# Kernel tuning notes

Hardware: AMD Instinct MI355X
Metric: run time of the kernel (lower is better)

## Reference

```python
import jax, jax.numpy as jnp
import numpy as np

B, H, W, C = 16, 192, 192, 128   # batch, height, width, d_inner
R = 16      # lora_rank (bottleneck width between lora_down and lora_up)
RK = 8      # internal LoRA rank = lora_rank // 2
NC = 5      # cache_size
SCALE = 1.0 / RK        # alpha / rank with alpha = 1.0
THRESH = 0.7            # similarity_threshold
EPS = 1e-8              # torch cosine_similarity eps


def _lora_paths(x, A1, B1, A2, B2):
    # lora_down: C -> RK -> R, lora_up: R -> RK -> C, each scaled by 1/RK (dropout off in eval)
    down = ((x @ A1) @ B1) * SCALE          # [B,H,W,R]
    up = ((down @ A2) @ B2) * SCALE         # [B,H,W,C]
    return down, up


def setup_inputs() -> dict:
    key = jax.random.key(0)
    ks = jax.random.split(key, 9)
    x = jax.random.normal(ks[0], (B, H, W, C), dtype=jnp.float32)
    A1 = (jax.random.normal(ks[1], (C, RK)) / np.sqrt(C)).astype(jnp.float32)
    B1 = (jax.random.normal(ks[2], (RK, R)) / np.sqrt(RK)).astype(jnp.float32)
    A2 = (jax.random.normal(ks[3], (R, RK)) / np.sqrt(R)).astype(jnp.float32)
    B2 = (jax.random.normal(ks[4], (RK, C)) / np.sqrt(RK)).astype(jnp.float32)
    W1 = (jax.random.normal(ks[5], (C + R, C)) / np.sqrt(C + R)).astype(jnp.float32)
    b1 = jnp.zeros((C,), dtype=jnp.float32)
    W2 = (jax.random.normal(ks[6], (C, C)) / np.sqrt(C)).astype(jnp.float32)
    b2 = jnp.zeros((C,), dtype=jnp.float32)
    cache_w = jnp.array(0.5, dtype=jnp.float32)
    # Build cache entries as noisy copies of x_lora[:NC] so the first NC batch
    # elements clear the 0.7 cosine threshold (fused branch) and the rest do not.
    _, xl = _lora_paths(x, A1, B1, A2, B2)
    noise = jax.random.normal(ks[7], (NC, H, W, C), dtype=jnp.float32) * (0.05 * jnp.std(xl))
    cache_feats = xl[:NC] + noise           # [NC,H,W,C]
    return {"x": x, "A1": A1, "B1": B1, "A2": A2, "B2": B2,
            "W1": W1, "b1": b1, "W2": W2, "b2": b2,
            "cache_w": cache_w, "cache_feats": cache_feats}


def reference(x, A1, B1, A2, B2, W1, b1, W2, b2, cache_w, cache_feats):
    down, x_lora = _lora_paths(x, A1, B1, A2, B2)   # [B,H,W,R], [B,H,W,C]
    # Per-channel cosine similarity over the HW axis, averaged over channels
    num = jnp.einsum('bhwc,nhwc->bnc', x_lora, cache_feats)        # [B,NC,C]
    xn = jnp.sqrt(jnp.sum(x_lora * x_lora, axis=(1, 2)))           # [B,C]
    cn = jnp.sqrt(jnp.sum(cache_feats * cache_feats, axis=(1, 2))) # [NC,C]
    denom = jnp.maximum(xn[:, None, :], EPS) * jnp.maximum(cn[None, :, :], EPS)
    sims = jnp.mean(num / denom, axis=-1)                          # [B,NC]
    best_idx = jnp.argmax(sims, axis=1)                            # first max, like list.index
    best_sim = jnp.max(sims, axis=1)
    best = cache_feats[best_idx]                                   # [B,H,W,C]
    # Gated blend with cached feature, then fusion MLP on concat([blend, lora_down])
    cw = jax.nn.sigmoid(cache_w)
    blend = cw * x_lora + (1.0 - cw) * best
    h = jnp.concatenate([blend, down], axis=-1) @ W1 + b1          # [B,H,W,C]
    fused = jax.nn.silu(h) @ W2 + b2
    mask = (best_sim > THRESH)[:, None, None, None]
    return jnp.where(mask, fused, x_lora)
```

## Files before the change

kernel.cpp:

```cpp
#include <hip/hip_runtime.h>
#include <math.h>

#define BATCH 16
#define HWPIX 36864
#define CCH 128
#define NCACHE 5
#define SCALE 0.125f
#define THRESH 0.7f
#define EPSV 1e-8f

typedef _Float16 f16;
typedef __attribute__((ext_vector_type(8))) _Float16 f16x8;
typedef __attribute__((ext_vector_type(4))) float f32x4;

__global__ __launch_bounds__(256) void kpre1(
    const float* __restrict__ A1, const float* __restrict__ B1,
    const float* __restrict__ A2, const float* __restrict__ B2,
    const float* __restrict__ W1, const float* __restrict__ W2,
    const float* __restrict__ cache_w,
    float* __restrict__ M1f, float* __restrict__ M12f,
    f16* __restrict__ M12h, f16* __restrict__ Qh, f16* __restrict__ W2h) {
  __shared__ float M1s[128 * 16];
  __shared__ float M2s[16 * 128];
  int t = threadIdx.x;
  int blk = blockIdx.x;
  for (int idx = t; idx < 2048; idx += 256) {
    int i = idx >> 4, r = idx & 15;
    float s = 0.f;
    for (int k = 0; k < 8; ++k) s += A1[i * 8 + k] * B1[k * 16 + r];
    s *= SCALE;
    M1s[idx] = s;
    if (blk == 0) M1f[idx] = s;
  }
  for (int idx = t; idx < 2048; idx += 256) {
    int r = idx >> 7, j = idx & 127;
    float s = 0.f;
    for (int k = 0; k < 8; ++k) s += A2[r * 8 + k] * B2[k * 128 + j];
    M2s[idx] = s * SCALE;
  }
  __syncthreads();
  for (int idx = blk * 2048 + t; idx < blk * 2048 + 2048; idx += 256) {
    int i = idx >> 7, j = idx & 127;
    float s = 0.f;
    for (int r = 0; r < 16; ++r) s += M1s[i * 16 + r] * M2s[r * 128 + j];
    M12f[idx] = s;
    M12h[(((i >> 3) * 128 + j) << 3) + (i & 7)] = (f16)s;
  }
  float cw = 1.f / (1.f + __expf(-cache_w[0]));
  float qs = 1.f - cw;
  for (int idx = blk * 2048 + t; idx < blk * 2048 + 2048; idx += 256) {
    int k = idx >> 7, n = idx & 127;
    int ci = (((k >> 3) * 128 + n) << 3) + (k & 7);
    Qh[ci] = (f16)(qs * W1[k * 128 + n]);
    W2h[ci] = (f16)W2[k * 128 + n];
  }
}

__global__ __launch_bounds__(256) void kpre2(
    const float* __restrict__ W1, const float* __restrict__ M1f,
    const float* __restrict__ M12f, const float* __restrict__ cache_w,
    f16* __restrict__ Ph) {
  int t = threadIdx.x;
  int k = blockIdx.x * 8 + (t >> 5);
  int n0 = (t & 31) * 4;
  float cw = 1.f / (1.f + __expf(-cache_w[0]));
  float sa[4] = {0, 0, 0, 0}, sb[4] = {0, 0, 0, 0};
  for (int tt = 0; tt < 128; ++tt) {
    float m = M12f[k * 128 + tt];
    const float* wr = &W1[tt * 128 + n0];
    sa[0] += m * wr[0]; sa[1] += m * wr[1]; sa[2] += m * wr[2]; sa[3] += m * wr[3];
  }
  for (int r = 0; r < 16; ++r) {
    float m = M1f[k * 16 + r];
    const float* wr = &W1[(128 + r) * 128 + n0];
    sb[0] += m * wr[0]; sb[1] += m * wr[1]; sb[2] += m * wr[2]; sb[3] += m * wr[3];
  }
  for (int u = 0; u < 4; ++u) {
    int n = n0 + u;
    Ph[(((k >> 3) * 128 + n) << 3) + (k & 7)] = (f16)(cw * sa[u] + sb[u]);
  }
}

__global__ __launch_bounds__(256, 3) void k2(
    const float* __restrict__ x, const float* __restrict__ cache,
    const f16* __restrict__ M12h, float* __restrict__ out,
    float* __restrict__ num, float* __restrict__ xn2, float* __restrict__ cn2) {
  __shared__ f16 Bs[16 * 128 * 8];
  __shared__ f16 XLb[64 * 132];
  int t = threadIdx.x;
  int chunk = blockIdx.x;
  int grp = blockIdx.y;
  long pb = (long)chunk * 64;
  {
    const uint4* src = (const uint4*)M12h;
    uint4* dst = (uint4*)Bs;
    for (int i = t; i < 2048; i += 256) dst[i] = src[i];
  }
  int lane = t & 63, w = t >> 6, l15 = lane & 15, q = lane >> 4;
  int arow = w * 16 + l15;
  int c = t & 127;
  bool hi = t >= 128;
  __syncthreads();

  for (int g = 0; g < 8; ++g) {
    int b = grp * 8 + g;
    const float* xb = x + ((long)b * HWPIX + pb) * CCH;
    f32x4 acc[8];
#pragma unroll
    for (int ni = 0; ni < 8; ++ni) acc[ni] = 0;
#pragma unroll
    for (int kk = 0; kk < 4; ++kk) {
      const float* ap = xb + arow * CCH + kk * 32 + q * 8;
      f32x4 a0 = *(const f32x4*)ap;
      f32x4 a1 = *(const f32x4*)(ap + 4);
      f16x8 a;
      a[0] = (f16)a0[0]; a[1] = (f16)a0[1]; a[2] = (f16)a0[2]; a[3] = (f16)a0[3];
      a[4] = (f16)a1[0]; a[5] = (f16)a1[1]; a[6] = (f16)a1[2]; a[7] = (f16)a1[3];
#pragma unroll
      for (int ni = 0; ni < 8; ++ni) {
        f16x8 bb = *(const f16x8*)&Bs[(((kk * 4 + q) * 128 + ni * 16 + l15)) << 3];
        acc[ni] = __builtin_amdgcn_mfma_f32_16x16x32_f16(a, bb, acc[ni], 0, 0, 0);
      }
    }
    __syncthreads();
    float* ob = out + ((long)b * HWPIX + pb) * CCH;
#pragma unroll
    for (int ni = 0; ni < 8; ++ni) {
      int cc = ni * 16 + l15;
#pragma unroll
      for (int r = 0; r < 4; ++r) {
        int p = w * 16 + q * 4 + r;
        float v = acc[ni][r];
        ob[(long)p * CCH + cc] = v;
        XLb[p * 132 + cc] = (f16)v;
      }
    }
    __syncthreads();
    {
      bool docn = (grp == 0) && (g == 0);
      const float* cb = cache + pb * CCH + c;
      float s0 = 0, s1 = 0, s2v = 0;
      float q0 = 0, q1 = 0, q2 = 0;
      if (!hi) {
#pragma unroll 4
        for (int p = 0; p < 64; ++p) {
          float xl = (float)XLb[p * 132 + c];
          float cv0 = cb[((long)0 * HWPIX + p) * CCH];
          float cv1 = cb[((long)1 * HWPIX + p) * CCH];
          float cv2 = cb[((long)2 * HWPIX + p) * CCH];
          s0 += xl * cv0; s1 += xl * cv1; s2v += xl * cv2;
          if (docn) { q0 += cv0 * cv0; q1 += cv1 * cv1; q2 += cv2 * cv2; }
        }
        atomicAdd(&num[((long)b * 5 + 0) * 128 + c], s0);
        atomicAdd(&num[((long)b * 5 + 1) * 128 + c], s1);
        atomicAdd(&num[((long)b * 5 + 2) * 128 + c], s2v);
        if (docn) {
          atomicAdd(&cn2[0 * 128 + c], q0);
          atomicAdd(&cn2[1 * 128 + c], q1);
          atomicAdd(&cn2[2 * 128 + c], q2);
        }
      } else {
#pragma unroll 4
        for (int p = 0; p < 64; ++p) {
          float xl = (float)XLb[p * 132 + c];
          float cv3 = cb[((long)3 * HWPIX + p) * CCH];
          float cv4 = cb[((long)4 * HWPIX + p) * CCH];
          s0 += xl * cv3; s1 += xl * cv4; s2v += xl * xl;
          if (docn) { q0 += cv3 * cv3; q1 += cv4 * cv4; }
        }
        atomicAdd(&num[((long)b * 5 + 3) * 128 + c], s0);
        atomicAdd(&num[((long)b * 5 + 4) * 128 + c], s1);
        atomicAdd(&xn2[b * 128 + c], s2v);
        if (docn) {
          atomicAdd(&cn2[3 * 128 + c], q0);
          atomicAdd(&cn2[4 * 128 + c], q1);
        }
      }
    }
  }
}

__global__ __launch_bounds__(128) void k3(
    const float* __restrict__ num, const float* __restrict__ xn2v,
    const float* __restrict__ cn2v, int* __restrict__ stats) {
  __shared__ float sims[16][5];
  int t = threadIdx.x;
  if (t < 80) {
    int b = t / 5, n = t % 5;
    float s = 0.f;
    for (int c = 0; c < 128; ++c) {
      float xn = sqrtf(xn2v[b * 128 + c]);
      float cn = sqrtf(cn2v[n * 128 + c]);
      s += num[(b * 5 + n) * 128 + c] / (fmaxf(xn, EPSV) * fmaxf(cn, EPSV));
    }
    sims[b][n] = s * (1.f / 128.f);
  }
  __syncthreads();
  if (t < 16) {
    float bv = -1e30f;
    int bi = 0;
    for (int n = 0; n < 5; ++n) {
      float v = sims[t][n];
      if (v > bv) { bv = v; bi = n; }
    }
    stats[t] = bi;
    stats[16 + t] = (bv > THRESH) ? 1 : 0;
  }
}

__global__ __launch_bounds__(256, 4) void k4(
    const float* __restrict__ x, const float* __restrict__ cache,
    const f16* __restrict__ Ph, const f16* __restrict__ Qh,
    const f16* __restrict__ W2h, const float* __restrict__ b1,
    const float* __restrict__ b2, const int* __restrict__ stats,
    float* __restrict__ out) {
  int b = blockIdx.y;
  if (!stats[16 + b]) return;
  __shared__ f16 As[16 * 64 * 8];
  int t = threadIdx.x;
  int bi = stats[b];
  long pb = (long)blockIdx.x * 64;
  const float* xb = x + ((long)b * HWPIX + pb) * CCH;
  const float* cb = cache + ((long)bi * HWPIX + pb) * CCH;
  int lane = t & 63, w = t >> 6, l15 = lane & 15, q = lane >> 4;
  int arow = w * 16 + l15;
  const uint4* Pf = (const uint4*)Ph;
  const uint4* Qf = (const uint4*)Qh;
  const uint4* Wf = (const uint4*)W2h;

  f32x4 acc[8];
#pragma unroll
  for (int ni = 0; ni < 8; ++ni) acc[ni] = 0;
#pragma unroll
  for (int kk = 0; kk < 4; ++kk) {
    const float* ap = xb + arow * CCH + kk * 32 + q * 8;
    f32x4 a0 = *(const f32x4*)ap;
    f32x4 a1 = *(const f32x4*)(ap + 4);
    f16x8 a;
    a[0] = (f16)a0[0]; a[1] = (f16)a0[1]; a[2] = (f16)a0[2]; a[3] = (f16)a0[3];
    a[4] = (f16)a1[0]; a[5] = (f16)a1[1]; a[6] = (f16)a1[2]; a[7] = (f16)a1[3];
#pragma unroll
    for (int ni = 0; ni < 8; ++ni) {
      uint4 bw = Pf[(kk * 4 + q) * 128 + ni * 16 + l15];
      acc[ni] = __builtin_amdgcn_mfma_f32_16x16x32_f16(a, *(const f16x8*)&bw,
                                                       acc[ni], 0, 0, 0);
    }
  }
#pragma unroll
  for (int kk = 0; kk < 4; ++kk) {
    const float* ap = cb + arow * CCH + kk * 32 + q * 8;
    f32x4 a0 = *(const f32x4*)ap;
    f32x4 a1 = *(const f32x4*)(ap + 4);
    f16x8 a;
    a[0] = (f16)a0[0]; a[1] = (f16)a0[1]; a[2] = (f16)a0[2]; a[3] = (f16)a0[3];
    a[4] = (f16)a1[0]; a[5] = (f16)a1[1]; a[6] = (f16)a1[2]; a[7] = (f16)a1[3];
#pragma unroll
    for (int ni = 0; ni < 8; ++ni) {
      uint4 bw = Qf[(kk * 4 + q) * 128 + ni * 16 + l15];
      acc[ni] = __builtin_amdgcn_mfma_f32_16x16x32_f16(a, *(const f16x8*)&bw,
                                                       acc[ni], 0, 0, 0);
    }
  }
#pragma unroll
  for (int ni = 0; ni < 8; ++ni) {
    int cc = ni * 16 + l15;
    float b1v = b1[cc];
#pragma unroll
    for (int r = 0; r < 4; ++r) {
      int p = w * 16 + q * 4 + r;
      float hv = acc[ni][r] + b1v;
      float sv = hv / (1.f + __expf(-hv));
      As[(((cc >> 3) * 64 + p) << 3) + (cc & 7)] = (f16)sv;
    }
  }
#pragma unroll
  for (int ni = 0; ni < 8; ++ni) acc[ni] = 0;
#pragma unroll
  for (int kk = 0; kk < 4; ++kk) {
    f16x8 a = *(const f16x8*)&As[((kk * 4 + q) * 64 + arow) << 3];
#pragma unroll
    for (int ni = 0; ni < 8; ++ni) {
      uint4 bw = Wf[(kk * 4 + q) * 128 + ni * 16 + l15];
      acc[ni] = __builtin_amdgcn_mfma_f32_16x16x32_f16(a, *(const f16x8*)&bw,
                                                       acc[ni], 0, 0, 0);
    }
  }
  float* ob = out + ((long)b * HWPIX + pb) * CCH;
#pragma unroll
  for (int ni = 0; ni < 8; ++ni) {
    int cc = ni * 16 + l15;
    float b2v = b2[cc];
#pragma unroll
    for (int r = 0; r < 4; ++r) {
      int p = w * 16 + q * 4 + r;
      ob[(long)p * CCH + cc] = acc[ni][r] + b2v;
    }
  }
}

extern "C" void kernel_launch(void* const* d_in, const int* in_sizes, int n_in,
                              void* d_out, int out_size, void* d_ws, size_t ws_size,
                              hipStream_t stream) {
  const float* x  = (const float*)d_in[0];
  const float* A1 = (const float*)d_in[1];
  const float* B1 = (const float*)d_in[2];
  const float* A2 = (const float*)d_in[3];
  const float* B2 = (const float*)d_in[4];
  const float* W1 = (const float*)d_in[5];
  const float* b1 = (const float*)d_in[6];
  const float* W2 = (const float*)d_in[7];
  const float* b2 = (const float*)d_in[8];
  const float* cache_w = (const float*)d_in[9];
  const float* cache   = (const float*)d_in[10];
  float* out = (float*)d_out;
  char* wsb = (char*)d_ws;
  float* num  = (float*)(wsb + 0);
  float* xn2  = (float*)(wsb + 40960);
  float* cn2  = (float*)(wsb + 49152);
  int*   stats= (int*)  (wsb + 51712);
  float* M1f  = (float*)(wsb + 51840);
  float* M12f = (float*)(wsb + 60032);
  f16*   M12h = (f16*)  (wsb + 125568);
  f16*   Ph   = (f16*)  (wsb + 158336);
  f16*   Qh   = (f16*)  (wsb + 191104);
  f16*   W2h  = (f16*)  (wsb + 223872);

  hipMemsetAsync(wsb, 0, 51712, stream);
  kpre1<<<8, 256, 0, stream>>>(A1, B1, A2, B2, W1, W2, cache_w, M1f, M12f, M12h, Qh, W2h);
  kpre2<<<16, 256, 0, stream>>>(W1, M1f, M12f, cache_w, Ph);
  k2<<<dim3(576, 2), 256, 0, stream>>>(x, cache, M12h, out, num, xn2, cn2);
  k3<<<1, 128, 0, stream>>>(num, xn2, cn2, stats);
  k4<<<dim3(576, 16), 256, 0, stream>>>(x, cache, Ph, Qh, W2h, b1, b2, stats, out);
}
```

Before: 886.2 us.

## Split x_lora GEMM from cosine-similarity reduction and reuse cache across batches

The fused k2 kernel, which computed x_lora and the cache similarity sums per batch while rereading the cache once per batch, is split in two. A GEMM-only kernel now writes x_lora to the output over a full batch grid, and a separate reduction kernel reads each cache pixel once and accumulates dot products for 8 batches at a time from the fp32 x_lora it reads back from global memory. This aims to cut redundant cache reads and atomics and to improve occupancy, at the cost of an extra pass that rereads x_lora from memory. In k4, the x and cache MFMA loops are also interleaved so their loads can overlap.

```diff
diff --git a/kernel.cpp b/kernel.cpp
--- a/kernel.cpp
+++ b/kernel.cpp
@@ -81,101 +81,99 @@
   }
 }
 
-__global__ __launch_bounds__(256, 3) void k2(
-    const float* __restrict__ x, const float* __restrict__ cache,
-    const f16* __restrict__ M12h, float* __restrict__ out,
-    float* __restrict__ num, float* __restrict__ xn2, float* __restrict__ cn2) {
-  __shared__ f16 Bs[16 * 128 * 8];
-  __shared__ f16 XLb[64 * 132];
-  int t = threadIdx.x;
-  int chunk = blockIdx.x;
-  int grp = blockIdx.y;
-  long pb = (long)chunk * 64;
-  {
-    const uint4* src = (const uint4*)M12h;
-    uint4* dst = (uint4*)Bs;
-    for (int i = t; i < 2048; i += 256) dst[i] = src[i];
-  }
+__global__ __launch_bounds__(256, 4) void k2(
+    const float* __restrict__ x, const f16* __restrict__ M12h,
+    float* __restrict__ out) {
+  int t = threadIdx.x;
+  long pb = (long)blockIdx.x * 64;
+  int b = blockIdx.y;
   int lane = t & 63, w = t >> 6, l15 = lane & 15, q = lane >> 4;
   int arow = w * 16 + l15;
+  const uint4* Bf = (const uint4*)M12h;
+  const float* xb = x + ((long)b * HWPIX + pb) * CCH;
+
+  f32x4 acc[8];
+#pragma unroll
+  for (int ni = 0; ni < 8; ++ni) acc[ni] = 0;
+#pragma unroll
+  for (int kk = 0; kk < 4; ++kk) {
+    const float* ap = xb + arow * CCH + kk * 32 + q * 8;
+    f32x4 a0 = *(const f32x4*)ap;
+    f32x4 a1 = *(const f32x4*)(ap + 4);
+    f16x8 a;
+    a[0] = (f16)a0[0]; a[1] = (f16)a0[1]; a[2] = (f16)a0[2]; a[3] = (f16)a0[3];
+    a[4] = (f16)a1[0]; a[5] = (f16)a1[1]; a[6] = (f16)a1[2]; a[7] = (f16)a1[3];
+#pragma unroll
+    for (int ni = 0; ni < 8; ++ni) {
+      uint4 bw = Bf[(kk * 4 + q) * 128 + ni * 16 + l15];
+      acc[ni] = __builtin_amdgcn_mfma_f32_16x16x32_f16(a, *(const f16x8*)&bw,
+                                                       acc[ni], 0, 0, 0);
+    }
+  }
+  float* ob = out + ((long)b * HWPIX + pb) * CCH;
+#pragma unroll
+  for (int ni = 0; ni < 8; ++ni) {
+    int c = ni * 16 + l15;
+#pragma unroll
+    for (int r = 0; r < 4; ++r) {
+      int p = w * 16 + q * 4 + r;
+      ob[(long)p * CCH + c] = acc[ni][r];
+    }
+  }
+}
+
+__global__ __launch_bounds__(256, 4) void k2b(
+    const float* __restrict__ xlr, const float* __restrict__ cache,
+    float* __restrict__ num, float* __restrict__ xn2, float* __restrict__ cn2) {
+  int t = threadIdx.x;
+  long pb = (long)blockIdx.x * 32;
   int c = t & 127;
-  bool hi = t >= 128;
-  __syncthreads();
-
-  for (int g = 0; g < 8; ++g) {
-    int b = grp * 8 + g;
-    const float* xb = x + ((long)b * HWPIX + pb) * CCH;
-    f32x4 acc[8];
-#pragma unroll
-    for (int ni = 0; ni < 8; ++ni) acc[ni] = 0;
-#pragma unroll
-    for (int kk = 0; kk < 4; ++kk) {
-      const float* ap = xb + arow * CCH + kk * 32 + q * 8;
-      f32x4 a0 = *(const f32x4*)ap;
-      f32x4 a1 = *(const f32x4*)(ap + 4);
-      f16x8 a;
-      a[0] = (f16)a0[0]; a[1] = (f16)a0[1]; a[2] = (f16)a0[2]; a[3] = (f16)a0[3];
-      a[4] = (f16)a1[0]; a[5] = (f16)a1[1]; a[6] = (f16)a1[2]; a[7] = (f16)a1[3];
-#pragma unroll
-      for (int ni = 0; ni < 8; ++ni) {
-        f16x8 bb = *(const f16x8*)&Bs[(((kk * 4 + q) * 128 + ni * 16 + l15)) << 3];
-        acc[ni] = __builtin_amdgcn_mfma_f32_16x16x32_f16(a, bb, acc[ni], 0, 0, 0);
+  int half = t >> 7;
+  const float* cb = cache + (pb + half * 16) * CCH + c;
+  const float* xb = xlr + (pb + half * 16) * CCH + c;
+
+  for (int bg = 0; bg < 2; ++bg) {
+    float sn[8][5];
+    float sx[8];
+    float sc[5];
+#pragma unroll
+    for (int bb = 0; bb < 8; ++bb) {
+      sx[bb] = 0.f;
+#pragma unroll
+      for (int n = 0; n < 5; ++n) sn[bb][n] = 0.f;
+    }
+#pragma unroll
+    for (int n = 0; n < 5; ++n) sc[n] = 0.f;
+
+#pragma unroll 4
+    for (int p = 0; p < 16; ++p) {
+      float cv[5];
+#pragma unroll
+      for (int n = 0; n < 5; ++n)
+        cv[n] = cb[((long)n * HWPIX + p) * CCH];
+#pragma unroll
+      for (int bb = 0; bb < 8; ++bb) {
+        float v = xb[((long)(bg * 8 + bb) * HWPIX + p) * CCH];
+        sx[bb] += v * v;
+#pragma unroll
+        for (int n = 0; n < 5; ++n) sn[bb][n] += v * cv[n];
       }
-    }
-    __syncthreads();
-    float* ob = out + ((long)b * HWPIX + pb) * CCH;
-#pragma unroll
-    for (int ni = 0; ni < 8; ++ni) {
-      int cc = ni * 16 + l15;
-#pragma unroll
-      for (int r = 0; r < 4; ++r) {
-        int p = w * 16 + q * 4 + r;
-        float v = acc[ni][r];
-        ob[(long)p * CCH + cc] = v;
-        XLb[p * 132 + cc] = (f16)v;
+      if (bg == 0) {
+#pragma unroll
+        for (int n = 0; n < 5; ++n) sc[n] += cv[n] * cv[n];
       }
     }
-    __syncthreads();
-    {
-      bool docn = (grp == 0) && (g == 0);
-      const float* cb = cache + pb * CCH + c;
-      float s0 = 0, s1 = 0, s2v = 0;
-      float q0 = 0, q1 = 0, q2 = 0;
-      if (!hi) {
-#pragma unroll 4
-        for (int p = 0; p < 64; ++p) {
-          float xl = (float)XLb[p * 132 + c];
-          float cv0 = cb[((long)0 * HWPIX + p) * CCH];
-          float cv1 = cb[((long)1 * HWPIX + p) * CCH];
-          float cv2 = cb[((long)2 * HWPIX + p) * CCH];
-          s0 += xl * cv0; s1 += xl * cv1; s2v += xl * cv2;
-          if (docn) { q0 += cv0 * cv0; q1 += cv1 * cv1; q2 += cv2 * cv2; }
-        }
-        atomicAdd(&num[((long)b * 5 + 0) * 128 + c], s0);
-        atomicAdd(&num[((long)b * 5 + 1) * 128 + c], s1);
-        atomicAdd(&num[((long)b * 5 + 2) * 128 + c], s2v);
-        if (docn) {
-          atomicAdd(&cn2[0 * 128 + c], q0);
-          atomicAdd(&cn2[1 * 128 + c], q1);
-          atomicAdd(&cn2[2 * 128 + c], q2);
-        }
-      } else {
-#pragma unroll 4
-        for (int p = 0; p < 64; ++p) {
-          float xl = (float)XLb[p * 132 + c];
-          float cv3 = cb[((long)3 * HWPIX + p) * CCH];
-          float cv4 = cb[((long)4 * HWPIX + p) * CCH];
-          s0 += xl * cv3; s1 += xl * cv4; s2v += xl * xl;
-          if (docn) { q0 += cv3 * cv3; q1 += cv4 * cv4; }
-        }
-        atomicAdd(&num[((long)b * 5 + 3) * 128 + c], s0);
-        atomicAdd(&num[((long)b * 5 + 4) * 128 + c], s1);
-        atomicAdd(&xn2[b * 128 + c], s2v);
-        if (docn) {
-          atomicAdd(&cn2[3 * 128 + c], q0);
-          atomicAdd(&cn2[4 * 128 + c], q1);
-        }
-      }
+#pragma unroll
+    for (int bb = 0; bb < 8; ++bb) {
+      int b = bg * 8 + bb;
+#pragma unroll
+      for (int n = 0; n < 5; ++n)
+        atomicAdd(&num[((long)b * 5 + n) * 128 + c], sn[bb][n]);
+      atomicAdd(&xn2[b * 128 + c], sx[bb]);
+    }
+    if (bg == 0) {
+#pragma unroll
+      for (int n = 0; n < 5; ++n) atomicAdd(&cn2[n * 128 + c], sc[n]);
     }
   }
 }
@@ -233,31 +231,24 @@
   for (int ni = 0; ni < 8; ++ni) acc[ni] = 0;
 #pragma unroll
   for (int kk = 0; kk < 4; ++kk) {
-    const float* ap = xb + arow * CCH + kk * 32 + q * 8;
-    f32x4 a0 = *(const f32x4*)ap;
-    f32x4 a1 = *(const f32x4*)(ap + 4);
-    f16x8 a;
-    a[0] = (f16)a0[0]; a[1] = (f16)a0[1]; a[2] = (f16)a0[2]; a[3] = (f16)a0[3];
-    a[4] = (f16)a1[0]; a[5] = (f16)a1[1]; a[6] = (f16)a1[2]; a[7] = (f16)a1[3];
+    const float* apx = xb + arow * CCH + kk * 32 + q * 8;
+    const float* apc = cb + arow * CCH + kk * 32 + q * 8;
+    f32x4 x0 = *(const f32x4*)apx;
+    f32x4 x1 = *(const f32x4*)(apx + 4);
+    f32x4 c0 = *(const f32x4*)apc;
+    f32x4 c1 = *(const f32x4*)(apc + 4);
+    f16x8 ax, ac;
+    ax[0] = (f16)x0[0]; ax[1] = (f16)x0[1]; ax[2] = (f16)x0[2]; ax[3] = (f16)x0[3];
+    ax[4] = (f16)x1[0]; ax[5] = (f16)x1[1]; ax[6] = (f16)x1[2]; ax[7] = (f16)x1[3];
+    ac[0] = (f16)c0[0]; ac[1] = (f16)c0[1]; ac[2] = (f16)c0[2]; ac[3] = (f16)c0[3];
+    ac[4] = (f16)c1[0]; ac[5] = (f16)c1[1]; ac[6] = (f16)c1[2]; ac[7] = (f16)c1[3];
 #pragma unroll
     for (int ni = 0; ni < 8; ++ni) {
-      uint4 bw = Pf[(kk * 4 + q) * 128 + ni * 16 + l15];
-      acc[ni] = __builtin_amdgcn_mfma_f32_16x16x32_f16(a, *(const f16x8*)&bw,
+      uint4 bp = Pf[(kk * 4 + q) * 128 + ni * 16 + l15];
+      uint4 bq = Qf[(kk * 4 + q) * 128 + ni * 16 + l15];
+      acc[ni] = __builtin_amdgcn_mfma_f32_16x16x32_f16(ax, *(const f16x8*)&bp,
                                                        acc[ni], 0, 0, 0);
-    }
-  }
-#pragma unroll
-  for (int kk = 0; kk < 4; ++kk) {
-    const float* ap = cb + arow * CCH + kk * 32 + q * 8;
-    f32x4 a0 = *(const f32x4*)ap;
-    f32x4 a1 = *(const f32x4*)(ap + 4);
-    f16x8 a;
-    a[0] = (f16)a0[0]; a[1] = (f16)a0[1]; a[2] = (f16)a0[2]; a[3] = (f16)a0[3];
-    a[4] = (f16)a1[0]; a[5] = (f16)a1[1]; a[6] = (f16)a1[2]; a[7] = (f16)a1[3];
-#pragma unroll
-    for (int ni = 0; ni < 8; ++ni) {
-      uint4 bw = Qf[(kk * 4 + q) * 128 + ni * 16 + l15];
-      acc[ni] = __builtin_amdgcn_mfma_f32_16x16x32_f16(a, *(const f16x8*)&bw,
+      acc[ni] = __builtin_amdgcn_mfma_f32_16x16x32_f16(ac, *(const f16x8*)&bq,
                                                        acc[ni], 0, 0, 0);
     }
   }
@@ -328,7 +319,8 @@
   hipMemsetAsync(wsb, 0, 51712, stream);
   kpre1<<<8, 256, 0, stream>>>(A1, B1, A2, B2, W1, W2, cache_w, M1f, M12f, M12h, Qh, W2h);
   kpre2<<<16, 256, 0, stream>>>(W1, M1f, M12f, cache_w, Ph);
-  k2<<<dim3(576, 2), 256, 0, stream>>>(x, cache, M12h, out, num, xn2, cn2);
+  k2<<<dim3(576, 16), 256, 0, stream>>>(x, M12h, out);
+  k2b<<<1152, 256, 0, stream>>>(out, cache, num, xn2, cn2);
   k3<<<1, 128, 0, stream>>>(num, xn2, cn2, stats);
   k4<<<dim3(576, 16), 256, 0, stream>>>(x, cache, Ph, Qh, W2h, b1, b2, stats, out);
 }
```

Result: no change. 891.4 us (+0.6%).
